# Kernel optimization log

Hardware: AMD Instinct MI355X
Metric: run time of the kernel (lower is better)

Reference implementation:

```python
import jax, jax.numpy as jnp
import numpy as np

EPS = 1e-5

def _bn_relu(x, gamma, beta):
    # BatchNorm2d (training-mode batch stats, biased var) + ReLU
    mean = jnp.mean(x, axis=(0, 2, 3), keepdims=True)
    var = jnp.var(x, axis=(0, 2, 3), keepdims=True)
    xn = (x - mean) * jax.lax.rsqrt(var + EPS)
    return jax.nn.relu(xn * gamma[None, :, None, None] + beta[None, :, None, None])


def setup_inputs() -> dict:
    key = jax.random.key(0)
    ks = jax.random.split(key, 8)
    plane, inter = 256, 128
    b, h, w = 2, 96, 96
    s_in = 1.0 / np.sqrt(plane)
    s_inter = 1.0 / np.sqrt(inter)
    s_cat = 1.0 / np.sqrt(2 * plane)
    return {
        "x": jax.random.normal(ks[0], (b, plane, h, w), dtype=jnp.float32),
        "Wk": jax.random.normal(ks[1], (inter, plane), dtype=jnp.float32) * s_in,
        "Wv": jax.random.normal(ks[2], (inter, plane), dtype=jnp.float32) * s_in,
        "Wq": jax.random.normal(ks[3], (inter, plane), dtype=jnp.float32) * s_in,
        "Wc1": jax.random.normal(ks[4], (plane, inter), dtype=jnp.float32) * s_inter,
        "gamma1": jnp.ones((plane,), dtype=jnp.float32),
        "beta1": jnp.zeros((plane,), dtype=jnp.float32),
        "Wout": jax.random.normal(ks[5], (plane, 2 * plane), dtype=jnp.float32) * s_cat,
        "gamma2": jnp.ones((plane,), dtype=jnp.float32),
        "beta2": jnp.zeros((plane,), dtype=jnp.float32),
    }


def reference(x, Wk, Wv, Wq, Wc1, gamma1, beta1, Wout, gamma2, beta2):
    b, C, h, w = x.shape
    N = h * w
    xf = x.reshape(b, C, N)               # [b, C, N]
    # 1x1 convs as channel GEMMs
    k = jnp.einsum('oc,bcn->bon', Wk, xf)  # [b, c, N]
    v = jnp.einsum('oc,bcn->bon', Wv, xf)  # [b, c, N]
    q = jnp.einsum('oc,bcn->bon', Wq, xf)  # [b, c, N]
    c = k.shape[1]
    scale = c ** (-0.5)
    # full NxN attention: sim = (q^T * scale) @ k
    sim = jnp.einsum('bcn,bcm->bnm', q * scale, k)   # [b, N, N]
    attn = jax.nn.softmax(sim, axis=-1)
    # gcn_feats = (attn @ v^T)^T  -> [b, c, N]
    gcn = jnp.einsum('bnm,bcm->bcn', attn, v).reshape(b, c, h, w)
    # conv1 + BN + ReLU
    gcn = _bn_relu(jnp.einsum('oc,bchw->bohw', Wc1, gcn), gamma1, beta1)
    # concat + out_conv + BN + ReLU
    cat = jnp.concatenate([x, gcn], axis=1)          # [b, 2C, h, w]
    out = _bn_relu(jnp.einsum('oc,bchw->bohw', Wout, cat), gamma2, beta2)
    return out
```

## Files before the change

kernel.cpp:

```cpp
#include <hip/hip_runtime.h>

typedef _Float16 h8_t __attribute__((ext_vector_type(8)));
typedef _Float16 h4_t __attribute__((ext_vector_type(4)));
typedef float f4_t __attribute__((ext_vector_type(4)));

#define NTOK 9216
#define CMID 128
#define NBATCH 2
#define KCHUNK 5
#define NKT 144
#define NSTAT 18432.0f


__device__ __forceinline__ h8_t cvt_f32x8_h8(const float* p) {
  f4_t a = *(const f4_t*)p, b = *(const f4_t*)(p + 4);
  h8_t h;
#pragma unroll
  for (int u = 0; u < 4; u++) { h[u] = (_Float16)a[u]; h[u + 4] = (_Float16)b[u]; }
  return h;
}

__global__ __launch_bounds__(256) void qkv_kernel(
    const float* __restrict__ x, const float* __restrict__ Wk,
    const float* __restrict__ Wv, const float* __restrict__ Wq,
    _Float16* __restrict__ Qt, _Float16* __restrict__ Kt,
    _Float16* __restrict__ V)
{
  const int b  = blockIdx.z;
  const int n0 = blockIdx.x * 64;
  const int o0 = blockIdx.y * 64;
  const int tid = threadIdx.x;
  const int wave = tid >> 6, lane = tid & 63, quad = lane >> 4, l16 = lane & 15;

  __shared__ _Float16 Wl[64][136];
  __shared__ _Float16 xl[64][136];
  __shared__ _Float16 Tt[128][68];

  const float* Wsel; int orow;
  if (o0 < 128)      { Wsel = Wq; orow = o0; }
  else if (o0 < 256) { Wsel = Wk; orow = o0 - 128; }
  else               { Wsel = Wv; orow = o0 - 256; }

  f4_t acc[4];
#pragma unroll
  for (int t = 0; t < 4; t++) acc[t] = (f4_t)(0.f);

  for (int kc = 0; kc < 256; kc += 128) {
    __syncthreads();
#pragma unroll
    for (int it = 0; it < 4; it++) {
      int idx = tid + it * 256;
      int row = idx >> 4, oc = idx & 15;
      *(h8_t*)&Wl[row][oc * 8] =
          cvt_f32x8_h8(&Wsel[(size_t)(orow + row) * 256 + kc + oc * 8]);
    }
#pragma unroll
    for (int it = 0; it < 8; it++) {
      int idx = tid + it * 256;
      int cl = idx >> 4, u = idx & 15;
      f4_t v = *(const f4_t*)&x[(size_t)(b * 256 + kc + cl) * NTOK + n0 + u * 4];
      h4_t h;
#pragma unroll
      for (int j = 0; j < 4; j++) h[j] = (_Float16)v[j];
      *(h4_t*)&Tt[cl][u * 4] = h;
    }
    __syncthreads();
#pragma unroll
    for (int it = 0; it < 4; it++) {
      int idx = tid + it * 256;
      int nl = idx & 63, oc = idx >> 6;
      h8_t h;
#pragma unroll
      for (int j = 0; j < 8; j++) h[j] = Tt[oc * 8 + j][nl];
      *(h8_t*)&xl[nl][oc * 8] = h;
    }
    __syncthreads();
#pragma unroll
    for (int ko = 0; ko < 4; ko++) {
      h8_t af = *(const h8_t*)&Wl[wave * 16 + l16][ko * 32 + quad * 8];
#pragma unroll
      for (int t = 0; t < 4; t++) {
        h8_t bf = *(const h8_t*)&xl[t * 16 + l16][ko * 32 + quad * 8];
        acc[t] = __builtin_amdgcn_mfma_f32_16x16x32_f16(af, bf, acc[t], 0, 0, 0);
      }
    }
  }

  const float qscale = 0.08838834764831845f * 1.4426950408889634f;
  if (o0 < 256) {
    _Float16* dst = (o0 < 128) ? Qt : Kt;
    const int od = ((o0 < 128) ? o0 : (o0 - 128)) + wave * 16 + quad * 4;
    const float s = (o0 < 128) ? qscale : 1.0f;
#pragma unroll
    for (int t = 0; t < 4; t++) {
      int n = n0 + t * 16 + l16;
      h4_t h;
#pragma unroll
      for (int r = 0; r < 4; r++) h[r] = (_Float16)(acc[t][r] * s);
      *(h4_t*)&dst[(size_t)(b * NTOK + n) * CMID + od] = h;
    }
  } else {
    const int c0 = o0 - 256 + wave * 16 + quad * 4;
#pragma unroll
    for (int t = 0; t < 4; t++) {
      int n = n0 + t * 16 + l16;
#pragma unroll
      for (int r = 0; r < 4; r++)
        V[(size_t)(b * CMID + c0 + r) * NTOK + n] = (_Float16)acc[t][r];
    }
  }
}

__global__ __launch_bounds__(256, 3) void flash_kernel(
    const _Float16* __restrict__ Qt, const _Float16* __restrict__ Kt,
    const _Float16* __restrict__ V,
    float* __restrict__ gcn_acc, float* __restrict__ l_acc)
{
  const int b  = blockIdx.z;
  const int kc = blockIdx.y;
  const int q0 = blockIdx.x * 128;
  const int tid = threadIdx.x;
  const int wave = tid >> 6, lane = tid & 63, quad = lane >> 4, l16 = lane & 15;

  __shared__ _Float16 Vl[128][72];
  __shared__ alignas(16) _Float16 UBuf[9216];
#define KL(r, c) UBuf[(r) * 136 + (c)]
#define PL(r, c) UBuf[(r) * 72 + (c)]

  h8_t qf[2][4];
#pragma unroll
  for (int qi = 0; qi < 2; qi++) {
    const _Float16* qp =
        Qt + (size_t)(b * NTOK + q0 + wave * 32 + qi * 16 + l16) * CMID;
#pragma unroll
    for (int ch = 0; ch < 4; ch++)
      qf[qi][ch] = *(const h8_t*)(qp + ch * 32 + quad * 8);
  }

  f4_t O[2][8];
#pragma unroll
  for (int qi = 0; qi < 2; qi++)
#pragma unroll
    for (int t = 0; t < 8; t++) O[qi][t] = (f4_t)(0.f);
  float l_r[2][4] = {{0.f, 0.f, 0.f, 0.f}, {0.f, 0.f, 0.f, 0.f}};

  const int t0 = (kc * NKT) / KCHUNK;
  const int t1 = ((kc + 1) * NKT) / KCHUNK;
  for (int k0 = t0 * 64; k0 < t1 * 64; k0 += 64) {
    __syncthreads();
    {
      const h8_t* src = (const h8_t*)(Kt + (size_t)(b * NTOK + k0) * CMID);
#pragma unroll
      for (int r = 0; r < 4; r++) {
        int idx = tid + r * 256;
        int row = idx >> 4, ch = idx & 15;
        *(h8_t*)&KL(row, ch * 8) = src[idx];
      }
      const _Float16* vs = V + (size_t)(b * CMID) * NTOK + k0;
#pragma unroll
      for (int r = 0; r < 4; r++) {
        int idx = tid + r * 256;
        int row = idx >> 3, ch = idx & 7;
        *(h8_t*)&Vl[row][ch * 8] = *(const h8_t*)(vs + (size_t)row * NTOK + ch * 8);
      }
    }
    __syncthreads();

    f4_t S[2][4];
#pragma unroll
    for (int qi = 0; qi < 2; qi++)
#pragma unroll
      for (int t = 0; t < 4; t++) S[qi][t] = (f4_t)(0.f);
#pragma unroll
    for (int ch = 0; ch < 4; ch++)
#pragma unroll
      for (int t = 0; t < 4; t++) {
        h8_t kf = *(const h8_t*)&KL(t * 16 + l16, ch * 32 + quad * 8);
        S[0][t] = __builtin_amdgcn_mfma_f32_16x16x32_f16(qf[0][ch], kf, S[0][t], 0, 0, 0);
        S[1][t] = __builtin_amdgcn_mfma_f32_16x16x32_f16(qf[1][ch], kf, S[1][t], 0, 0, 0);
      }
    __syncthreads();

#pragma unroll
    for (int qi = 0; qi < 2; qi++)
#pragma unroll
      for (int t = 0; t < 4; t++)
#pragma unroll
        for (int r = 0; r < 4; r++) {
          float p = exp2f(S[qi][t][r] - 8.0f);
          l_r[qi][r] += p;
          PL(wave * 32 + qi * 16 + quad * 4 + r, t * 16 + l16) = (_Float16)p;
        }

#pragma unroll
    for (int ch = 0; ch < 2; ch++) {
      h8_t pf0 = *(const h8_t*)&PL(wave * 32 + l16, ch * 32 + quad * 8);
      h8_t pf1 = *(const h8_t*)&PL(wave * 32 + 16 + l16, ch * 32 + quad * 8);
#pragma unroll
      for (int t = 0; t < 8; t++) {
        h8_t vf = *(const h8_t*)&Vl[t * 16 + l16][ch * 32 + quad * 8];
        O[0][t] = __builtin_amdgcn_mfma_f32_16x16x32_f16(pf0, vf, O[0][t], 0, 0, 0);
        O[1][t] = __builtin_amdgcn_mfma_f32_16x16x32_f16(pf1, vf, O[1][t], 0, 0, 0);
      }
    }
  }
#undef KL
#undef PL

#pragma unroll
  for (int qi = 0; qi < 2; qi++)
#pragma unroll
    for (int r = 0; r < 4; r++) {
      float v = l_r[qi][r];
      v += __shfl_xor(v, 1); v += __shfl_xor(v, 2);
      v += __shfl_xor(v, 4); v += __shfl_xor(v, 8);
      if (l16 == 0)
        atomicAdd(&l_acc[b * NTOK + q0 + wave * 32 + qi * 16 + quad * 4 + r], v);
    }
#pragma unroll
  for (int qi = 0; qi < 2; qi++)
#pragma unroll
    for (int t = 0; t < 8; t++)
#pragma unroll
      for (int r = 0; r < 4; r++)
        atomicAdd(&gcn_acc[(size_t)(b * NTOK + q0 + wave * 32 + qi * 16 + quad * 4 + r)
                               * CMID + t * 16 + l16],
                  O[qi][t][r]);
}

__global__ __launch_bounds__(256) void conv1_kernel(
    const float* __restrict__ gcn_acc, const float* __restrict__ l_acc,
    const float* __restrict__ Wc1,
    _Float16* __restrict__ g1t, float* __restrict__ sum1, float* __restrict__ sq1)
{
  const int b  = blockIdx.z;
  const int n0 = blockIdx.x * 64;
  const int o0 = blockIdx.y * 64;
  const int tid = threadIdx.x;
  const int wave = tid >> 6, lane = tid & 63, quad = lane >> 4, l16 = lane & 15;

  __shared__ _Float16 Gl[64][136];
  __shared__ _Float16 Wcl[64][136];
  __shared__ float rl[64];
  __shared__ float ssum[64], ssq[64];

  if (tid < 64) {
    rl[tid] = 1.0f / l_acc[b * NTOK + n0 + tid];
    ssum[tid] = 0.f; ssq[tid] = 0.f;
  }
  __syncthreads();

#pragma unroll
  for (int it = 0; it < 4; it++) {
    int idx = tid + it * 256;
    int n = idx >> 4, oc = idx & 15;
    const float* gp = &gcn_acc[(size_t)(b * NTOK + n0 + n) * CMID + oc * 8];
    float s = rl[n];
    f4_t a = *(const f4_t*)gp, c = *(const f4_t*)(gp + 4);
    h8_t h;
#pragma unroll
    for (int u = 0; u < 4; u++) {
      h[u] = (_Float16)(a[u] * s);
      h[u + 4] = (_Float16)(c[u] * s);
    }
    *(h8_t*)&Gl[n][oc * 8] = h;
  }
#pragma unroll
  for (int it = 0; it < 4; it++) {
    int idx = tid + it * 256;
    int row = idx >> 4, oc = idx & 15;
    *(h8_t*)&Wcl[row][oc * 8] =
        cvt_f32x8_h8(&Wc1[(size_t)(o0 + row) * 128 + oc * 8]);
  }
  __syncthreads();

  f4_t acc[4];
#pragma unroll
  for (int t = 0; t < 4; t++) acc[t] = (f4_t)(0.f);
#pragma unroll
  for (int ko = 0; ko < 4; ko++) {
    h8_t af = *(const h8_t*)&Gl[wave * 16 + l16][ko * 32 + quad * 8];
#pragma unroll
    for (int t = 0; t < 4; t++) {
      h8_t bf = *(const h8_t*)&Wcl[t * 16 + l16][ko * 32 + quad * 8];
      acc[t] = __builtin_amdgcn_mfma_f32_16x16x32_f16(af, bf, acc[t], 0, 0, 0);
    }
  }

#pragma unroll
  for (int t = 0; t < 4; t++) {
    int ol = t * 16 + l16;
    float ls = 0.f, lq = 0.f;
#pragma unroll
    for (int r = 0; r < 4; r++) {
      float v = acc[t][r];
      ls += v; lq += v * v;
      g1t[(size_t)(b * NTOK + n0 + wave * 16 + quad * 4 + r) * 256 + o0 + ol] =
          (_Float16)v;
    }
    atomicAdd(&ssum[ol], ls);
    atomicAdd(&ssq[ol], lq);
  }
  __syncthreads();
  if (tid < 64) {
    atomicAdd(&sum1[o0 + tid], ssum[tid]);
    atomicAdd(&sq1[o0 + tid], ssq[tid]);
  }
}

__global__ __launch_bounds__(256) void out_kernel(
    const float* __restrict__ x, const _Float16* __restrict__ g1t,
    const float* __restrict__ Wout,
    const float* __restrict__ sum1, const float* __restrict__ sq1,
    const float* __restrict__ gamma1, const float* __restrict__ beta1,
    _Float16* __restrict__ out2, float* __restrict__ sum2, float* __restrict__ sq2)
{
  const int b  = blockIdx.z;
  const int n0 = blockIdx.x * 64;
  const int o0 = blockIdx.y * 64;
  const int tid = threadIdx.x;
  const int wave = tid >> 6, lane = tid & 63, quad = lane >> 4, l16 = lane & 15;

  __shared__ _Float16 Wol[64][136];
  __shared__ _Float16 Bl[64][136];
  __shared__ _Float16 Tt[128][68];
  __shared__ _Float16 scs[256], shs[256];
  __shared__ float ssum[64], ssq[64];

  {
    float m = sum1[tid] * (1.f / NSTAT);
    float var = sq1[tid] * (1.f / NSTAT) - m * m;
    float s = gamma1[tid] * rsqrtf(var + 1e-5f);
    scs[tid] = (_Float16)s;
    shs[tid] = (_Float16)(beta1[tid] - m * s);
  }
  if (tid < 64) { ssum[tid] = 0.f; ssq[tid] = 0.f; }

  f4_t acc[4];
#pragma unroll
  for (int t = 0; t < 4; t++) acc[t] = (f4_t)(0.f);

  for (int kc = 0; kc < 512; kc += 128) {
    __syncthreads();
#pragma unroll
    for (int it = 0; it < 4; it++) {
      int idx = tid + it * 256;
      int row = idx >> 4, oc = idx & 15;
      *(h8_t*)&Wol[row][oc * 8] =
          cvt_f32x8_h8(&Wout[(size_t)(o0 + row) * 512 + kc + oc * 8]);
    }
    if (kc < 256) {
#pragma unroll
      for (int it = 0; it < 8; it++) {
        int idx = tid + it * 256;
        int cl = idx >> 4, u = idx & 15;
        f4_t v = *(const f4_t*)&x[(size_t)(b * 256 + kc + cl) * NTOK + n0 + u * 4];
        h4_t h;
#pragma unroll
        for (int j = 0; j < 4; j++) h[j] = (_Float16)v[j];
        *(h4_t*)&Tt[cl][u * 4] = h;
      }
      __syncthreads();
#pragma unroll
      for (int it = 0; it < 4; it++) {
        int idx = tid + it * 256;
        int nl = idx & 63, oc = idx >> 6;
        h8_t h;
#pragma unroll
        for (int j = 0; j < 8; j++) h[j] = Tt[oc * 8 + j][nl];
        *(h8_t*)&Bl[nl][oc * 8] = h;
      }
    } else {
#pragma unroll
      for (int it = 0; it < 4; it++) {
        int idx = tid + it * 256;
        int n = idx >> 4, oc = idx & 15;
        int cg = kc - 256 + oc * 8;
        h8_t g = *(const h8_t*)&g1t[(size_t)(b * NTOK + n0 + n) * 256 + cg];
        h8_t h;
#pragma unroll
        for (int u = 0; u < 8; u++) {
          float t = (float)scs[cg + u] * (float)g[u] + (float)shs[cg + u];
          h[u] = (_Float16)(t > 0.f ? t : 0.f);
        }
        *(h8_t*)&Bl[n][oc * 8] = h;
      }
    }
    __syncthreads();
#pragma unroll
    for (int ko = 0; ko < 4; ko++) {
      h8_t af = *(const h8_t*)&Wol[wave * 16 + l16][ko * 32 + quad * 8];
#pragma unroll
      for (int t = 0; t < 4; t++) {
        h8_t bf = *(const h8_t*)&Bl[t * 16 + l16][ko * 32 + quad * 8];
        acc[t] = __builtin_amdgcn_mfma_f32_16x16x32_f16(af, bf, acc[t], 0, 0, 0);
      }
    }
  }

#pragma unroll
  for (int r = 0; r < 4; r++) {
    int o = o0 + wave * 16 + quad * 4 + r;
    float ls = 0.f, lq = 0.f;
#pragma unroll
    for (int t = 0; t < 4; t++) {
      float v = acc[t][r];
      ls += v; lq += v * v;
      out2[(size_t)(b * 256 + o) * NTOK + n0 + t * 16 + l16] = (_Float16)v;
    }
    atomicAdd(&ssum[wave * 16 + quad * 4 + r], ls);
    atomicAdd(&ssq[wave * 16 + quad * 4 + r], lq);
  }
  __syncthreads();
  if (tid < 64) {
    atomicAdd(&sum2[o0 + tid], ssum[tid]);
    atomicAdd(&sq2[o0 + tid], ssq[tid]);
  }
}

__global__ __launch_bounds__(256) void bn2_kernel(
    const _Float16* __restrict__ out2, const float* __restrict__ sum2,
    const float* __restrict__ sq2, const float* __restrict__ gamma2,
    const float* __restrict__ beta2, float* __restrict__ out)
{
  size_t i = ((size_t)blockIdx.x * 256 + threadIdx.x) * 8;
  int o = (int)((i / NTOK) & 255);
  float m = sum2[o] * (1.f / NSTAT);
  float var = sq2[o] * (1.f / NSTAT) - m * m;
  float s = gamma2[o] * rsqrtf(var + 1e-5f);
  float h = beta2[o] - m * s;
  h8_t v = *(const h8_t*)&out2[i];
  f4_t r0, r1;
#pragma unroll
  for (int u = 0; u < 4; u++) {
    float t0 = s * (float)v[u] + h;
    float t1 = s * (float)v[u + 4] + h;
    r0[u] = t0 > 0.f ? t0 : 0.f;
    r1[u] = t1 > 0.f ? t1 : 0.f;
  }
  *(f4_t*)&out[i] = r0;
  *(f4_t*)&out[i + 4] = r1;
}

extern "C" void kernel_launch(void* const* d_in, const int* in_sizes, int n_in,
                              void* d_out, int out_size, void* d_ws, size_t ws_size,
                              hipStream_t stream) {
  const float* x      = (const float*)d_in[0];
  const float* Wk     = (const float*)d_in[1];
  const float* Wv     = (const float*)d_in[2];
  const float* Wq     = (const float*)d_in[3];
  const float* Wc1    = (const float*)d_in[4];
  const float* gamma1 = (const float*)d_in[5];
  const float* beta1  = (const float*)d_in[6];
  const float* Wout   = (const float*)d_in[7];
  const float* gamma2 = (const float*)d_in[8];
  const float* beta2  = (const float*)d_in[9];
  float* out = (float*)d_out;

  char* ws = (char*)d_ws;
  float* sum1 = (float*)(ws + 0 * 1024);
  float* sq1  = (float*)(ws + 1 * 1024);
  float* sum2 = (float*)(ws + 2 * 1024);
  float* sq2  = (float*)(ws + 3 * 1024);

  const size_t R = (size_t)NBATCH * NTOK * CMID * 2;
  char* base = ws + 8 * 1024;
  _Float16* Qt   = (_Float16*)(base + 0 * R);
  _Float16* Kt   = (_Float16*)(base + 1 * R);
  _Float16* V    = (_Float16*)(base + 2 * R);
  _Float16* g1t  = (_Float16*)(base + 0 * R);
  _Float16* out2 = (_Float16*)(base + 2 * R);

  float* gcn_acc = (float*)d_out;
  float* l_acc   = (float*)((char*)d_out + (size_t)NBATCH * NTOK * CMID * 4);

  hipMemsetAsync(sum1, 0, 4 * 1024, stream);
  hipMemsetAsync(gcn_acc, 0,
                 (size_t)NBATCH * NTOK * CMID * 4 + (size_t)NBATCH * NTOK * 4,
                 stream);

  qkv_kernel<<<dim3(144, 6, 2), 256, 0, stream>>>(x, Wk, Wv, Wq, Qt, Kt, V);
  flash_kernel<<<dim3(72, KCHUNK, 2), 256, 0, stream>>>(Qt, Kt, V, gcn_acc, l_acc);
  conv1_kernel<<<dim3(144, 4, 2), 256, 0, stream>>>(gcn_acc, l_acc, Wc1, g1t, sum1, sq1);
  out_kernel<<<dim3(144, 4, 2), 256, 0, stream>>>(x, g1t, Wout, sum1, sq1, gamma1, beta1,
                                                  out2, sum2, sq2);
  bn2_kernel<<<2304, 256, 0, stream>>>(out2, sum2, sq2, gamma2, beta2, out);
}
```

Measured before the change: 339.0 us.

## Prefetch K/V tiles into registers and XOR-swizzle shared memory layouts

The flash kernel now loads the next K and V tiles into registers while the current tile's softmax and PV MFMAs run, hiding global latency behind compute. Separate K, V and P buffers replace the aliased buffer, which removes one barrier per iteration. Padded LDS rows are replaced by XOR-swizzled layouts to avoid bank conflicts. The costs are extra registers for the prefetch buffers and more LDS (48KB total), which may lower occupancy below the requested 3 blocks per CU.

```diff
diff --git a/kernel.cpp b/kernel.cpp
--- a/kernel.cpp
+++ b/kernel.cpp
@@ -122,10 +122,9 @@
   const int tid = threadIdx.x;
   const int wave = tid >> 6, lane = tid & 63, quad = lane >> 4, l16 = lane & 15;
 
-  __shared__ _Float16 Vl[128][72];
-  __shared__ alignas(16) _Float16 UBuf[9216];
-#define KL(r, c) UBuf[(r) * 136 + (c)]
-#define PL(r, c) UBuf[(r) * 72 + (c)]
+  __shared__ alignas(16) _Float16 Kl[64 * 128];
+  __shared__ alignas(16) _Float16 Vl[128 * 64];
+  __shared__ alignas(16) _Float16 Pl[128 * 64];
 
   h8_t qf[2][4];
 #pragma unroll
@@ -146,23 +145,34 @@
 
   const int t0 = (kc * NKT) / KCHUNK;
   const int t1 = ((kc + 1) * NKT) / KCHUNK;
-  for (int k0 = t0 * 64; k0 < t1 * 64; k0 += 64) {
-    __syncthreads();
-    {
-      const h8_t* src = (const h8_t*)(Kt + (size_t)(b * NTOK + k0) * CMID);
-#pragma unroll
-      for (int r = 0; r < 4; r++) {
-        int idx = tid + r * 256;
-        int row = idx >> 4, ch = idx & 15;
-        *(h8_t*)&KL(row, ch * 8) = src[idx];
-      }
-      const _Float16* vs = V + (size_t)(b * CMID) * NTOK + k0;
-#pragma unroll
-      for (int r = 0; r < 4; r++) {
-        int idx = tid + r * 256;
-        int row = idx >> 3, ch = idx & 7;
-        *(h8_t*)&Vl[row][ch * 8] = *(const h8_t*)(vs + (size_t)row * NTOK + ch * 8);
-      }
+  const int k_end = t1 * 64;
+
+  h8_t kpre[4], vpre[4];
+  {
+    const h8_t* src = (const h8_t*)(Kt + (size_t)(b * NTOK + t0 * 64) * CMID);
+#pragma unroll
+    for (int r = 0; r < 4; r++) kpre[r] = src[tid + r * 256];
+    const _Float16* vs = V + (size_t)(b * CMID) * NTOK + t0 * 64;
+#pragma unroll
+    for (int r = 0; r < 4; r++) {
+      int idx = tid + r * 256;
+      vpre[r] = *(const h8_t*)(vs + (size_t)(idx >> 3) * NTOK + (idx & 7) * 8);
+    }
+  }
+
+  for (int k0 = t0 * 64; k0 < k_end; k0 += 64) {
+    __syncthreads();
+#pragma unroll
+    for (int r = 0; r < 4; r++) {
+      int idx = tid + r * 256;
+      int row = idx >> 4, ch = idx & 15;
+      *(h8_t*)&Kl[row * 128 + ((ch ^ row) & 15) * 8] = kpre[r];
+    }
+#pragma unroll
+    for (int r = 0; r < 4; r++) {
+      int idx = tid + r * 256;
+      int row = idx >> 3, ch = idx & 7;
+      *(h8_t*)&Vl[row * 64 + ((ch ^ row) & 7) * 8] = vpre[r];
     }
     __syncthreads();
 
@@ -175,11 +185,11 @@
     for (int ch = 0; ch < 4; ch++)
 #pragma unroll
       for (int t = 0; t < 4; t++) {
-        h8_t kf = *(const h8_t*)&KL(t * 16 + l16, ch * 32 + quad * 8);
+        int chunk = ch * 4 + quad;
+        h8_t kf = *(const h8_t*)&Kl[(t * 16 + l16) * 128 + ((chunk ^ l16) & 15) * 8];
         S[0][t] = __builtin_amdgcn_mfma_f32_16x16x32_f16(qf[0][ch], kf, S[0][t], 0, 0, 0);
         S[1][t] = __builtin_amdgcn_mfma_f32_16x16x32_f16(qf[1][ch], kf, S[1][t], 0, 0, 0);
       }
-    __syncthreads();
 
 #pragma unroll
     for (int qi = 0; qi < 2; qi++)
@@ -189,23 +199,38 @@
         for (int r = 0; r < 4; r++) {
           float p = exp2f(S[qi][t][r] - 8.0f);
           l_r[qi][r] += p;
-          PL(wave * 32 + qi * 16 + quad * 4 + r, t * 16 + l16) = (_Float16)p;
+          int q = wave * 32 + qi * 16 + quad * 4 + r;
+          int key = t * 16 + l16;
+          Pl[q * 64 + (((key >> 3) ^ q) & 7) * 8 + (key & 7)] = (_Float16)p;
         }
 
+    if (k0 + 64 < k_end) {
+      const h8_t* src = (const h8_t*)(Kt + (size_t)(b * NTOK + k0 + 64) * CMID);
+#pragma unroll
+      for (int r = 0; r < 4; r++) kpre[r] = src[tid + r * 256];
+      const _Float16* vs = V + (size_t)(b * CMID) * NTOK + k0 + 64;
+#pragma unroll
+      for (int r = 0; r < 4; r++) {
+        int idx = tid + r * 256;
+        vpre[r] = *(const h8_t*)(vs + (size_t)(idx >> 3) * NTOK + (idx & 7) * 8);
+      }
+    }
+
 #pragma unroll
     for (int ch = 0; ch < 2; ch++) {
-      h8_t pf0 = *(const h8_t*)&PL(wave * 32 + l16, ch * 32 + quad * 8);
-      h8_t pf1 = *(const h8_t*)&PL(wave * 32 + 16 + l16, ch * 32 + quad * 8);
+      int chunk = ch * 4 + quad;
+      int qa = wave * 32 + l16, qb = wave * 32 + 16 + l16;
+      h8_t pf0 = *(const h8_t*)&Pl[qa * 64 + ((chunk ^ (l16 & 7)) & 7) * 8];
+      h8_t pf1 = *(const h8_t*)&Pl[qb * 64 + ((chunk ^ (l16 & 7)) & 7) * 8];
 #pragma unroll
       for (int t = 0; t < 8; t++) {
-        h8_t vf = *(const h8_t*)&Vl[t * 16 + l16][ch * 32 + quad * 8];
+        int c = t * 16 + l16;
+        h8_t vf = *(const h8_t*)&Vl[c * 64 + ((chunk ^ (c & 7)) & 7) * 8];
         O[0][t] = __builtin_amdgcn_mfma_f32_16x16x32_f16(pf0, vf, O[0][t], 0, 0, 0);
         O[1][t] = __builtin_amdgcn_mfma_f32_16x16x32_f16(pf1, vf, O[1][t], 0, 0, 0);
       }
     }
   }
-#undef KL
-#undef PL
 
 #pragma unroll
   for (int qi = 0; qi < 2; qi++)
```

After: 704.5 us. 108% more time.
